# Performance work log

Measured on AMD Instinct MI355X. Metric: run time of the kernel, lower is better.

Reference implementation:

```python
import jax, jax.numpy as jnp
import numpy as np

H = 768
R = 24


def setup_inputs() -> dict:
    key = jax.random.key(0)
    ks = jax.random.split(key, 9)
    B, S = 4, 256
    hidden = jax.random.normal(ks[0], (B, S, H), dtype=jnp.float32)
    # ConcatHandshaking fc: Linear(2H -> H); torch weight shape (out,in)=(H,2H)
    fc_w = jax.random.normal(ks[1], (H, 2 * H), dtype=jnp.float32) * (1.0 / np.sqrt(2 * H))
    fc_b = jnp.zeros((H,), dtype=jnp.float32)
    # h2t: Linear(H -> 2)
    h2t_w = jax.random.normal(ks[2], (2, H), dtype=jnp.float32) * (1.0 / np.sqrt(H))
    h2t_b = jnp.zeros((2,), dtype=jnp.float32)
    # h2h / t2t TaggingProjector: R independent Linear(H -> 3), batched as (R,3,H)
    h2h_w = jax.random.normal(ks[3], (R, 3, H), dtype=jnp.float32) * (1.0 / np.sqrt(H))
    h2h_b = jnp.zeros((R, 3), dtype=jnp.float32)
    t2t_w = jax.random.normal(ks[4], (R, 3, H), dtype=jnp.float32) * (1.0 / np.sqrt(H))
    t2t_b = jnp.zeros((R, 3), dtype=jnp.float32)
    return {
        "hidden": hidden,
        "fc_w": fc_w, "fc_b": fc_b,
        "h2t_w": h2t_w, "h2t_b": h2t_b,
        "h2h_w": h2h_w, "h2h_b": h2h_b,
        "t2t_w": t2t_w, "t2t_b": t2t_b,
    }


def _handshaking(hidden, fc_w, fc_b):
    # hidden: (B, S, H). Pairs (i, j) with i <= j in row-major (torch loop) order.
    S = hidden.shape[1]
    idx_i, idx_j = jnp.triu_indices(S)  # each (P,), P = S(S+1)/2
    # concat([h_i, h_j]) @ W^T == h_i @ Wl^T + h_j @ Wr^T  (avoids (B,P,2H) buffer)
    Wl = fc_w[:, :H]  # (H, H)
    Wr = fc_w[:, H:]  # (H, H)
    left = jnp.einsum('bsh,oh->bso', hidden, Wl)   # (B, S, H)
    right = jnp.einsum('bsh,oh->bso', hidden, Wr)  # (B, S, H)
    hs = jnp.tanh(left[:, idx_i, :] + right[:, idx_j, :] + fc_b)  # (B, P, H)
    return hs


def reference(hidden, fc_w, fc_b, h2t_w, h2t_b, h2h_w, h2h_b, t2t_w, t2t_b):
    hs = _handshaking(hidden, fc_w, fc_b)  # (B, P, H)
    # h2t: plain Linear(H->2), logits (no softmax in original)
    h2t = jnp.einsum('bph,oh->bpo', hs, h2t_w) + h2t_b  # (B, P, 2)
    # TaggingProjector: batched per-relation Linear(H->3), then softmax over tags
    h2h = jax.nn.softmax(jnp.einsum('bph,rth->brpt', hs, h2h_w) + h2h_b[None, :, None, :], axis=-1)
    t2t = jax.nn.softmax(jnp.einsum('bph,rth->brpt', hs, t2t_w) + t2t_b[None, :, None, :], axis=-1)
    return (h2t, h2h, t2t)
```

## Files before the change

kernel.cpp:

```cpp
#include <hip/hip_runtime.h>
#include <hip/hip_bf16.h>

#define H 768
#define SEQ 256
#define NPAIR 32896
#define NTOT 131584
#define NOUTP 160
#define OFF_H2H 263168u
#define OFF_T2T 9737216u

#define N_BPK 122880
#define N_FCW 1179648
#define SCL 2.8853900817779268f

#define CH 32
#define NCH 24
#define BSLOT 12288
#define SLAB_STR 166

typedef short bf16x8 __attribute__((ext_vector_type(8)));
typedef float f32x4 __attribute__((ext_vector_type(4)));

__device__ __forceinline__ float tanh_s(float xs) {
    float e = __builtin_amdgcn_exp2f(xs);
    return fmaf(-2.0f, __builtin_amdgcn_rcpf(e + 1.0f), 1.0f);
}
__device__ __forceinline__ float bf_lo(int w){ return __uint_as_float(((unsigned)w) << 16); }
__device__ __forceinline__ float bf_hi(int w){ return __uint_as_float(((unsigned)w) & 0xffff0000u); }
__device__ __forceinline__ float bfu(unsigned short u){ return __uint_as_float(((unsigned)u) << 16); }
__device__ __forceinline__ int cvtpk(float lo, float hi) {
    int r;
    asm("v_cvt_pk_bf16_f32 %0, %1, %2" : "=v"(r) : "v"(lo), "v"(hi));
    return r;
}
__device__ __forceinline__ unsigned short bf16r(float x){
    unsigned int u = __float_as_uint(x);
    u += 0x7fffu + ((u >> 16) & 1u);
    return (unsigned short)(u >> 16);
}
__device__ __forceinline__ bf16x8 tanh_frag(int4 lv, int4 rv) {
    int4 st;
    st.x = cvtpk(tanh_s(bf_lo(lv.x) + bf_lo(rv.x)), tanh_s(bf_hi(lv.x) + bf_hi(rv.x)));
    st.y = cvtpk(tanh_s(bf_lo(lv.y) + bf_lo(rv.y)), tanh_s(bf_hi(lv.y) + bf_hi(rv.y)));
    st.z = cvtpk(tanh_s(bf_lo(lv.z) + bf_lo(rv.z)), tanh_s(bf_hi(lv.z) + bf_hi(rv.z)));
    st.w = cvtpk(tanh_s(bf_lo(lv.w) + bf_lo(rv.w)), tanh_s(bf_hi(lv.w) + bf_hi(rv.w)));
    return __builtin_bit_cast(bf16x8, st);
}

typedef const __attribute__((address_space(1))) unsigned int* as1_u32p;
typedef __attribute__((address_space(3))) unsigned int* as3_u32p;
__device__ __forceinline__ void gload_lds16(const void* g, void* l) {
    __builtin_amdgcn_global_load_lds((as1_u32p)g, (as3_u32p)l, 16, 0, 0);
}

__device__ __forceinline__ int row_start(int i) { return i * SEQ - (i * (i - 1)) / 2; }
__device__ __forceinline__ void pair_ij(int p, int& oi, int& oj) {
    double disc = 263169.0 - 8.0 * (double)p;
    int i = (int)((513.0 - sqrt(disc)) * 0.5);
    if (i > 0 && row_start(i) > p) --i;
    while (row_start(i + 1) <= p) ++i;
    oi = i;
    oj = i + (p - row_start(i));
}
__device__ __forceinline__ int batch_of(int g) {
    return (g >= 3 * NPAIR) ? 3 : (g >= 2 * NPAIR) ? 2 : (g >= NPAIR) ? 1 : 0;
}

__global__ __launch_bounds__(256) void pack_kernel(
    const float* __restrict__ h2t_w, const float* __restrict__ h2h_w,
    const float* __restrict__ t2t_w, const float* __restrict__ h2t_b,
    const float* __restrict__ h2h_b, const float* __restrict__ t2t_b,
    const float* __restrict__ fc_w,
    unsigned short* __restrict__ Bpk, unsigned short* __restrict__ fcwb,
    float* __restrict__ bc)
{
    int idx = blockIdx.x * 256 + threadIdx.x;
    if (idx < N_BPK) {
        int j = idx & 7, lane = (idx >> 3) & 63, rest = idx >> 9;
        int f = rest % 10, c = rest / 10;
        int n = f * 16 + (lane & 15);
        int k = c * CH + ((lane >> 4) << 3) + j;
        float v = 0.f;
        if (n < 2)        v = h2t_w[n * H + k];
        else if (n < 74)  v = h2h_w[(n - 2) * H + k];
        else if (n < 146) v = t2t_w[(n - 74) * H + k];
        Bpk[c * 6144 + (idx - c * 5120)] = bf16r(v);
    } else if (idx < N_BPK + N_FCW) {
        int q = idx - N_BPK;
        int n = q / H, k = q % H;
        float v = (n < H) ? fc_w[(size_t)n * 2 * H + k]
                          : fc_w[(size_t)(n - H) * 2 * H + H + k];
        fcwb[q] = bf16r(v);
    } else if (idx < N_BPK + N_FCW + NOUTP) {
        int q = idx - N_BPK - N_FCW;
        float v = 0.f;
        if (q < 2)        v = h2t_b[q];
        else if (q < 74)  v = h2h_b[q - 2];
        else if (q < 146) v = t2t_b[q - 74];
        bc[q] = v;
    }
}

__global__ __launch_bounds__(256, 2) void lr_mfma(
    const float* __restrict__ hidden, const unsigned short* __restrict__ fcwb,
    const float* __restrict__ fc_b,
    unsigned short* __restrict__ LB, unsigned short* __restrict__ RB)
{
    __shared__ __align__(16) char sm[24576];
    const int tid = threadIdx.x, l = tid & 63, w = tid >> 6;
    const int wm = w >> 1, wn = w & 1;
    const int m0 = blockIdx.x * 64, n0 = blockIdx.y * 128;
    f32x4 acc[2][4] = {};
    for (int c = 0; c < 12; ++c) {
        const int k0 = c * 64;
        #pragma unroll
        for (int it = 0; it < 2; ++it) {
            int idx = tid + it * 256;
            int row = idx >> 3, k8 = idx & 7;
            const float4* src = reinterpret_cast<const float4*>(hidden + (size_t)(m0 + row) * H + k0 + k8 * 8);
            float4 a = src[0], bq = src[1];
            int4 st;
            st.x = cvtpk(a.x, a.y);  st.y = cvtpk(a.z, a.w);
            st.z = cvtpk(bq.x, bq.y); st.w = cvtpk(bq.z, bq.w);
            *reinterpret_cast<int4*>(sm + row * 128 + ((k8 * 16) ^ ((row & 7) << 4))) = st;
        }
        #pragma unroll
        for (int it = 0; it < 4; ++it) {
            int idx = tid + it * 256;
            int row = idx >> 3, k8 = idx & 7;
            *reinterpret_cast<int4*>(sm + 8192 + row * 128 + ((k8 * 16) ^ ((row & 7) << 4))) =
                *reinterpret_cast<const int4*>(fcwb + (size_t)(n0 + row) * H + k0 + k8 * 8);
        }
        __syncthreads();
        #pragma unroll
        for (int kk = 0; kk < 2; ++kk) {
            const int sl = kk * 4 + (l >> 4);
            const int swz = (l & 7) << 4;
            bf16x8 af[2], bfr[4];
            #pragma unroll
            for (int a = 0; a < 2; ++a) {
                int row = 32 * wm + 16 * a + (l & 15);
                af[a] = *reinterpret_cast<const bf16x8*>(sm + row * 128 + ((sl * 16) ^ swz));
            }
            #pragma unroll
            for (int f = 0; f < 4; ++f) {
                int row = 64 * wn + 16 * f + (l & 15);
                bfr[f] = *reinterpret_cast<const bf16x8*>(sm + 8192 + row * 128 + ((sl * 16) ^ swz));
            }
            #pragma unroll
            for (int a = 0; a < 2; ++a)
                #pragma unroll
                for (int f = 0; f < 4; ++f)
                    acc[a][f] = __builtin_amdgcn_mfma_f32_16x16x32_bf16(af[a], bfr[f], acc[a][f], 0, 0, 0);
        }
        __syncthreads();
    }
    #pragma unroll
    for (int a = 0; a < 2; ++a)
        #pragma unroll
        for (int f = 0; f < 4; ++f)
            #pragma unroll
            for (int r = 0; r < 4; ++r) {
                int row = m0 + 32 * wm + 16 * a + 4 * (l >> 4) + r;
                int col = n0 + 64 * wn + 16 * f + (l & 15);
                float v = acc[a][f][r];
                if (n0 < H) LB[(size_t)row * H + col] = bf16r((v + fc_b[col]) * SCL);
                else        RB[(size_t)row * H + (col - H)] = bf16r(v * SCL);
            }
}

__global__ __launch_bounds__(256, 4) void pair_mfma(
    const unsigned short* __restrict__ LB, const unsigned short* __restrict__ RB,
    const unsigned short* __restrict__ Bpk, const float* __restrict__ bc,
    float* __restrict__ out)
{
    __shared__ __align__(16) char sm[25216];
    int*   iOf  = reinterpret_cast<int*>(sm);
    int*   jOf  = reinterpret_cast<int*>(sm + 256);
    float* bc_s = reinterpret_cast<float*>(sm + 24576);

    const int tid = threadIdx.x, l = tid & 63, w = tid >> 6;
    const int g0 = blockIdx.x * 64;
    const int b = batch_of(g0);
    const int p0 = g0 - b * NPAIR;

    if (tid < 64) {
        int i, j; pair_ij(p0 + tid, i, j);
        iOf[tid] = (b * SEQ + i) * H;
        jOf[tid] = (b * SEQ + j) * H;
    }
    if (tid < NOUTP) bc_s[tid] = bc[tid];
    __syncthreads();

    const int row = 16 * w + (l & 15);
    const unsigned short* lp = LB + iOf[row] + ((l >> 4) << 3);
    const unsigned short* rp = RB + jOf[row] + ((l >> 4) << 3);
    __syncthreads();

    const char* bp = reinterpret_cast<const char*>(Bpk) + w * 1024 + l * 16;
    const int d0 = w * 1024;

    f32x4 acc[10] = {};
    int4 lv[3], rv[3];

    {
        gload_lds16(bp,        sm + d0);
        gload_lds16(bp + 4096, sm + 4096 + d0);
        gload_lds16(bp + 8192, sm + 8192 + d0);
        __builtin_amdgcn_sched_barrier(0);
    }
    lv[0] = *reinterpret_cast<const int4*>(lp);
    rv[0] = *reinterpret_cast<const int4*>(rp);
    lv[1] = *reinterpret_cast<const int4*>(lp + CH);
    rv[1] = *reinterpret_cast<const int4*>(rp + CH);
    asm volatile("s_waitcnt vmcnt(4)" ::: "memory");
    __builtin_amdgcn_s_barrier();
    __builtin_amdgcn_sched_barrier(0);

    #pragma unroll
    for (int c = 0; c < NCH - 2; ++c) {
        char* bufn = sm + (((c + 1) & 1) ? BSLOT : 0);
        const char* bn = bp + (c + 1) * BSLOT;
        gload_lds16(bn,        bufn + d0);
        gload_lds16(bn + 4096, bufn + 4096 + d0);
        gload_lds16(bn + 8192, bufn + 8192 + d0);
        __builtin_amdgcn_sched_barrier(0);
        bf16x8 a0 = tanh_frag(lv[c % 3], rv[c % 3]);
        const int co = (c + 2) * CH;
        lv[(c + 2) % 3] = *reinterpret_cast<const int4*>(lp + co);
        rv[(c + 2) % 3] = *reinterpret_cast<const int4*>(rp + co);
        const char* bufc = sm + ((c & 1) ? BSLOT : 0);
        #pragma unroll
        for (int f = 0; f < 10; ++f) {
            bf16x8 bfr = *reinterpret_cast<const bf16x8*>(bufc + (f * 64 + l) * 16);
            acc[f] = __builtin_amdgcn_mfma_f32_16x16x32_bf16(a0, bfr, acc[f], 0, 0, 0);
        }
        asm volatile("s_waitcnt vmcnt(2)" ::: "memory");
        __builtin_amdgcn_s_barrier();
        __builtin_amdgcn_sched_barrier(0);
    }
    {
        char* bufn = sm + BSLOT;
        const char* bn = bp + 23 * BSLOT;
        gload_lds16(bn,        bufn + d0);
        gload_lds16(bn + 4096, bufn + 4096 + d0);
        gload_lds16(bn + 8192, bufn + 8192 + d0);
        __builtin_amdgcn_sched_barrier(0);
        bf16x8 a0 = tanh_frag(lv[22 % 3], rv[22 % 3]);
        const char* bufc = sm;
        #pragma unroll
        for (int f = 0; f < 10; ++f) {
            bf16x8 bfr = *reinterpret_cast<const bf16x8*>(bufc + (f * 64 + l) * 16);
            acc[f] = __builtin_amdgcn_mfma_f32_16x16x32_bf16(a0, bfr, acc[f], 0, 0, 0);
        }
        asm volatile("s_waitcnt vmcnt(0)" ::: "memory");
        __builtin_amdgcn_s_barrier();
        __builtin_amdgcn_sched_barrier(0);
    }
    {
        bf16x8 a0 = tanh_frag(lv[23 % 3], rv[23 % 3]);
        const char* bufc = sm + BSLOT;
        #pragma unroll
        for (int f = 0; f < 10; ++f) {
            bf16x8 bfr = *reinterpret_cast<const bf16x8*>(bufc + (f * 64 + l) * 16);
            acc[f] = __builtin_amdgcn_mfma_f32_16x16x32_bf16(a0, bfr, acc[f], 0, 0, 0);
        }
    }
    asm volatile("s_waitcnt lgkmcnt(0)" ::: "memory");
    __builtin_amdgcn_s_barrier();

    unsigned short* slab = reinterpret_cast<unsigned short*>(sm);
    #pragma unroll
    for (int f = 0; f < 10; ++f)
        #pragma unroll
        for (int r = 0; r < 4; ++r) {
            int rw = 16 * w + 4 * (l >> 4) + r;
            slab[rw * SLAB_STR + f * 16 + (l & 15)] = bf16r(acc[f][r]);
        }
    __syncthreads();

    if (tid < 128) {
        int pr = tid >> 1, tt = tid & 1;
        float val = bfu(slab[pr * SLAB_STR + tt]) + bc_s[tt];
        __builtin_nontemporal_store(val, &out[(size_t)(g0 + pr) * 2 + tt]);
    }
    #pragma unroll
    for (int it = 0; it < 12; ++it) {
        int item = it * 256 + tid;
        int pr = item & 63, rr = item >> 6;
        int p = p0 + pr;
        int ob = 2 + rr * 3;
        const unsigned short* sp = slab + pr * SLAB_STR + ob;
        float l0 = bfu(sp[0]) + bc_s[ob + 0];
        float l1 = bfu(sp[1]) + bc_s[ob + 1];
        float l2 = bfu(sp[2]) + bc_s[ob + 2];
        float mx = fmaxf(l0, fmaxf(l1, l2));
        float e0 = __expf(l0 - mx), e1 = __expf(l1 - mx), e2 = __expf(l2 - mx);
        float inv = __fdividef(1.0f, e0 + e1 + e2);
        size_t base = (rr < 24)
            ? (size_t)OFF_H2H + ((size_t)(b * 24 + rr) * NPAIR + p) * 3
            : (size_t)OFF_T2T + ((size_t)(b * 24 + rr - 24) * NPAIR + p) * 3;
        __builtin_nontemporal_store(e0 * inv, &out[base + 0]);
        __builtin_nontemporal_store(e1 * inv, &out[base + 1]);
        __builtin_nontemporal_store(e2 * inv, &out[base + 2]);
    }
}

extern "C" void kernel_launch(void* const* d_in, const int* in_sizes, int n_in,
                              void* d_out, int out_size, void* d_ws, size_t ws_size,
                              hipStream_t stream) {
    const float* hidden = (const float*)d_in[0];
    const float* fc_w   = (const float*)d_in[1];
    const float* fc_b   = (const float*)d_in[2];
    const float* h2t_w  = (const float*)d_in[3];
    const float* h2t_b  = (const float*)d_in[4];
    const float* h2h_w  = (const float*)d_in[5];
    const float* h2h_b  = (const float*)d_in[6];
    const float* t2t_w  = (const float*)d_in[7];
    const float* t2t_b  = (const float*)d_in[8];

    char* wsb = (char*)d_ws;
    unsigned short* LBw  = (unsigned short*)(wsb);
    unsigned short* RBw  = (unsigned short*)(wsb + 1572864);
    unsigned short* Bpk  = (unsigned short*)(wsb + 3145728);
    unsigned short* fcwb = (unsigned short*)(wsb + 3440640);
    float*          bc   = (float*)        (wsb + 5799936);

    float* out = (float*)d_out;

    pack_kernel<<<(N_BPK + N_FCW + NOUTP + 255) / 256, 256, 0, stream>>>(
        h2t_w, h2h_w, t2t_w, h2t_b, h2h_b, t2t_b, fc_w, Bpk, fcwb, bc);
    lr_mfma<<<dim3(16, 12), 256, 0, stream>>>(hidden, fcwb, fc_b, LBw, RBw);
    pair_mfma<<<NTOT / 64, 256, 0, stream>>>(LBw, RBw, Bpk, bc, out);
}
```

Measured before the change: 93.89 us.

## Precompute exp2 of left/right projections so pair tanh needs only a multiply

The left and right projection kernel now stores exp2 of the scaled projections. The pair kernel then computes tanh(l+r) as 1-2/(e_l*e_r+1), which replaces one exp per pair element with a multiply. The fc_w bf16 packing pass is removed: lr_mfma reads fp32 fc_w directly and converts it on the fly, using a smaller 64-wide N tile and twice as many blocks. Storing exponentials in bf16 changes the rounding behaviour, and very large values may saturate to infinity, though the rcp-based formula still gives tanh=1 there.

```diff
diff --git a/kernel.cpp b/kernel.cpp
--- a/kernel.cpp
+++ b/kernel.cpp
@@ -10,7 +10,6 @@
 #define OFF_T2T 9737216u
 
 #define N_BPK 122880
-#define N_FCW 1179648
 #define SCL 2.8853900817779268f
 
 #define CH 32
@@ -21,10 +20,6 @@
 typedef short bf16x8 __attribute__((ext_vector_type(8)));
 typedef float f32x4 __attribute__((ext_vector_type(4)));
 
-__device__ __forceinline__ float tanh_s(float xs) {
-    float e = __builtin_amdgcn_exp2f(xs);
-    return fmaf(-2.0f, __builtin_amdgcn_rcpf(e + 1.0f), 1.0f);
-}
 __device__ __forceinline__ float bf_lo(int w){ return __uint_as_float(((unsigned)w) << 16); }
 __device__ __forceinline__ float bf_hi(int w){ return __uint_as_float(((unsigned)w) & 0xffff0000u); }
 __device__ __forceinline__ float bfu(unsigned short u){ return __uint_as_float(((unsigned)u) << 16); }
@@ -38,12 +33,16 @@
     u += 0x7fffu + ((u >> 16) & 1u);
     return (unsigned short)(u >> 16);
 }
-__device__ __forceinline__ bf16x8 tanh_frag(int4 lv, int4 rv) {
+__device__ __forceinline__ float tanh_e(float el, float er) {
+    float e = el * er;
+    return fmaf(-2.0f, __builtin_amdgcn_rcpf(e + 1.0f), 1.0f);
+}
+__device__ __forceinline__ bf16x8 prod_frag(int4 lv, int4 rv) {
     int4 st;
-    st.x = cvtpk(tanh_s(bf_lo(lv.x) + bf_lo(rv.x)), tanh_s(bf_hi(lv.x) + bf_hi(rv.x)));
-    st.y = cvtpk(tanh_s(bf_lo(lv.y) + bf_lo(rv.y)), tanh_s(bf_hi(lv.y) + bf_hi(rv.y)));
-    st.z = cvtpk(tanh_s(bf_lo(lv.z) + bf_lo(rv.z)), tanh_s(bf_hi(lv.z) + bf_hi(rv.z)));
-    st.w = cvtpk(tanh_s(bf_lo(lv.w) + bf_lo(rv.w)), tanh_s(bf_hi(lv.w) + bf_hi(rv.w)));
+    st.x = cvtpk(tanh_e(bf_lo(lv.x), bf_lo(rv.x)), tanh_e(bf_hi(lv.x), bf_hi(rv.x)));
+    st.y = cvtpk(tanh_e(bf_lo(lv.y), bf_lo(rv.y)), tanh_e(bf_hi(lv.y), bf_hi(rv.y)));
+    st.z = cvtpk(tanh_e(bf_lo(lv.z), bf_lo(rv.z)), tanh_e(bf_hi(lv.z), bf_hi(rv.z)));
+    st.w = cvtpk(tanh_e(bf_lo(lv.w), bf_lo(rv.w)), tanh_e(bf_hi(lv.w), bf_hi(rv.w)));
     return __builtin_bit_cast(bf16x8, st);
 }
 
@@ -70,9 +69,7 @@
     const float* __restrict__ h2t_w, const float* __restrict__ h2h_w,
     const float* __restrict__ t2t_w, const float* __restrict__ h2t_b,
     const float* __restrict__ h2h_b, const float* __restrict__ t2t_b,
-    const float* __restrict__ fc_w,
-    unsigned short* __restrict__ Bpk, unsigned short* __restrict__ fcwb,
-    float* __restrict__ bc)
+    unsigned short* __restrict__ Bpk, float* __restrict__ bc)
 {
     int idx = blockIdx.x * 256 + threadIdx.x;
     if (idx < N_BPK) {
@@ -85,14 +82,8 @@
         else if (n < 74)  v = h2h_w[(n - 2) * H + k];
         else if (n < 146) v = t2t_w[(n - 74) * H + k];
         Bpk[c * 6144 + (idx - c * 5120)] = bf16r(v);
-    } else if (idx < N_BPK + N_FCW) {
+    } else if (idx < N_BPK + NOUTP) {
         int q = idx - N_BPK;
-        int n = q / H, k = q % H;
-        float v = (n < H) ? fc_w[(size_t)n * 2 * H + k]
-                          : fc_w[(size_t)(n - H) * 2 * H + H + k];
-        fcwb[q] = bf16r(v);
-    } else if (idx < N_BPK + N_FCW + NOUTP) {
-        int q = idx - N_BPK - N_FCW;
         float v = 0.f;
         if (q < 2)        v = h2t_b[q];
         else if (q < 74)  v = h2h_b[q - 2];
@@ -102,15 +93,15 @@
 }
 
 __global__ __launch_bounds__(256, 2) void lr_mfma(
-    const float* __restrict__ hidden, const unsigned short* __restrict__ fcwb,
+    const float* __restrict__ hidden, const float* __restrict__ fc_w,
     const float* __restrict__ fc_b,
     unsigned short* __restrict__ LB, unsigned short* __restrict__ RB)
 {
-    __shared__ __align__(16) char sm[24576];
+    __shared__ __align__(16) char sm[16384];
     const int tid = threadIdx.x, l = tid & 63, w = tid >> 6;
     const int wm = w >> 1, wn = w & 1;
-    const int m0 = blockIdx.x * 64, n0 = blockIdx.y * 128;
-    f32x4 acc[2][4] = {};
+    const int m0 = blockIdx.x * 64, n0 = blockIdx.y * 64;
+    f32x4 acc[2][2] = {};
     for (int c = 0; c < 12; ++c) {
         const int k0 = c * 64;
         #pragma unroll
@@ -125,32 +116,39 @@
             *reinterpret_cast<int4*>(sm + row * 128 + ((k8 * 16) ^ ((row & 7) << 4))) = st;
         }
         #pragma unroll
-        for (int it = 0; it < 4; ++it) {
+        for (int it = 0; it < 2; ++it) {
             int idx = tid + it * 256;
             int row = idx >> 3, k8 = idx & 7;
-            *reinterpret_cast<int4*>(sm + 8192 + row * 128 + ((k8 * 16) ^ ((row & 7) << 4))) =
-                *reinterpret_cast<const int4*>(fcwb + (size_t)(n0 + row) * H + k0 + k8 * 8);
+            const float* fsrc = (n0 < H)
+                ? fc_w + (size_t)(n0 + row) * (2 * H) + k0 + k8 * 8
+                : fc_w + (size_t)(n0 - H + row) * (2 * H) + H + k0 + k8 * 8;
+            const float4* src = reinterpret_cast<const float4*>(fsrc);
+            float4 a = src[0], bq = src[1];
+            int4 st;
+            st.x = cvtpk(a.x, a.y);  st.y = cvtpk(a.z, a.w);
+            st.z = cvtpk(bq.x, bq.y); st.w = cvtpk(bq.z, bq.w);
+            *reinterpret_cast<int4*>(sm + 8192 + row * 128 + ((k8 * 16) ^ ((row & 7) << 4))) = st;
         }
         __syncthreads();
         #pragma unroll
         for (int kk = 0; kk < 2; ++kk) {
             const int sl = kk * 4 + (l >> 4);
             const int swz = (l & 7) << 4;
-            bf16x8 af[2], bfr[4];
+            bf16x8 af[2], bfr[2];
             #pragma unroll
             for (int a = 0; a < 2; ++a) {
                 int row = 32 * wm + 16 * a + (l & 15);
                 af[a] = *reinterpret_cast<const bf16x8*>(sm + row * 128 + ((sl * 16) ^ swz));
             }
             #pragma unroll
-            for (int f = 0; f < 4; ++f) {
-                int row = 64 * wn + 16 * f + (l & 15);
+            for (int f = 0; f < 2; ++f) {
+                int row = 32 * wn + 16 * f + (l & 15);
                 bfr[f] = *reinterpret_cast<const bf16x8*>(sm + 8192 + row * 128 + ((sl * 16) ^ swz));
             }
             #pragma unroll
             for (int a = 0; a < 2; ++a)
                 #pragma unroll
-                for (int f = 0; f < 4; ++f)
+                for (int f = 0; f < 2; ++f)
                     acc[a][f] = __builtin_amdgcn_mfma_f32_16x16x32_bf16(af[a], bfr[f], acc[a][f], 0, 0, 0);
         }
         __syncthreads();
@@ -158,14 +156,16 @@
     #pragma unroll
     for (int a = 0; a < 2; ++a)
         #pragma unroll
-        for (int f = 0; f < 4; ++f)
+        for (int f = 0; f < 2; ++f)
             #pragma unroll
             for (int r = 0; r < 4; ++r) {
                 int row = m0 + 32 * wm + 16 * a + 4 * (l >> 4) + r;
-                int col = n0 + 64 * wn + 16 * f + (l & 15);
+                int col = n0 + 32 * wn + 16 * f + (l & 15);
                 float v = acc[a][f][r];
-                if (n0 < H) LB[(size_t)row * H + col] = bf16r((v + fc_b[col]) * SCL);
-                else        RB[(size_t)row * H + (col - H)] = bf16r(v * SCL);
+                if (n0 < H) LB[(size_t)row * H + col] =
+                    bf16r(__builtin_amdgcn_exp2f((v + fc_b[col]) * SCL));
+                else        RB[(size_t)row * H + (col - H)] =
+                    bf16r(__builtin_amdgcn_exp2f(v * SCL));
             }
 }
 
@@ -225,7 +225,7 @@
         gload_lds16(bn + 4096, bufn + 4096 + d0);
         gload_lds16(bn + 8192, bufn + 8192 + d0);
         __builtin_amdgcn_sched_barrier(0);
-        bf16x8 a0 = tanh_frag(lv[c % 3], rv[c % 3]);
+        bf16x8 a0 = prod_frag(lv[c % 3], rv[c % 3]);
         const int co = (c + 2) * CH;
         lv[(c + 2) % 3] = *reinterpret_cast<const int4*>(lp + co);
         rv[(c + 2) % 3] = *reinterpret_cast<const int4*>(rp + co);
@@ -246,7 +246,7 @@
         gload_lds16(bn + 4096, bufn + 4096 + d0);
         gload_lds16(bn + 8192, bufn + 8192 + d0);
         __builtin_amdgcn_sched_barrier(0);
-        bf16x8 a0 = tanh_frag(lv[22 % 3], rv[22 % 3]);
+        bf16x8 a0 = prod_frag(lv[22 % 3], rv[22 % 3]);
         const char* bufc = sm;
         #pragma unroll
         for (int f = 0; f < 10; ++f) {
@@ -258,7 +258,7 @@
         __builtin_amdgcn_sched_barrier(0);
     }
     {
-        bf16x8 a0 = tanh_frag(lv[23 % 3], rv[23 % 3]);
+        bf16x8 a0 = prod_frag(lv[23 % 3], rv[23 % 3]);
         const char* bufc = sm + BSLOT;
         #pragma unroll
         for (int f = 0; f < 10; ++f) {
@@ -323,13 +323,12 @@
     unsigned short* LBw  = (unsigned short*)(wsb);
     unsigned short* RBw  = (unsigned short*)(wsb + 1572864);
     unsigned short* Bpk  = (unsigned short*)(wsb + 3145728);
-    unsigned short* fcwb = (unsigned short*)(wsb + 3440640);
-    float*          bc   = (float*)        (wsb + 5799936);
+    float*          bc   = (float*)        (wsb + 3440640);
 
     float* out = (float*)d_out;
 
-    pack_kernel<<<(N_BPK + N_FCW + NOUTP + 255) / 256, 256, 0, stream>>>(
-        h2t_w, h2h_w, t2t_w, h2t_b, h2h_b, t2t_b, fc_w, Bpk, fcwb, bc);
-    lr_mfma<<<dim3(16, 12), 256, 0, stream>>>(hidden, fcwb, fc_b, LBw, RBw);
+    pack_kernel<<<(N_BPK + NOUTP + 255) / 256, 256, 0, stream>>>(
+        h2t_w, h2h_w, t2t_w, h2t_b, h2h_b, t2t_b, Bpk, bc);
+    lr_mfma<<<dim3(16, 24), 256, 0, stream>>>(hidden, fc_w, fc_b, LBw, RBw);
     pair_mfma<<<NTOT / 64, 256, 0, stream>>>(LBw, RBw, Bpk, bc, out);
 }
```

New measurement: 89.30 us. -4.9%, faster.
